# Kernel tuning notes

Measured on AMD Instinct MI355X. Metric: run time of the kernel, lower is better.

## Reference

```python
import jax, jax.numpy as jnp
import numpy as np

B, N, H, W = 1, 256, 32, 32
C_LIDAR, C_RGB, K, S = 64, 64, 16, 3
MLP3 = [128, 64, 64]


def _l2norm(x, eps=1e-12):
    n = jnp.linalg.norm(x, axis=-1, keepdims=True)
    return x / jnp.maximum(n, eps)


def _cal_sim(src, dst):
    # src [B,N,C], dst [B,M,C] -> [B,N,M,2] (cosine sim normalized two ways)
    s = _l2norm(src)
    d = _l2norm(dst)
    sim = jnp.einsum('bmc,bnc->bmn', d, s)  # [B,M,N]
    dst_src = sim / (jnp.max(sim, axis=2, keepdims=True) + 1e-10)
    src_dst = jnp.swapaxes(sim, 1, 2)       # [B,N,M]
    src_dst = src_dst / (jnp.max(src_dst, axis=2, keepdims=True) + 1e-6)
    return jnp.stack([src_dst, jnp.swapaxes(dst_src, 1, 2)], axis=-1)


def _mlp(x, layers):
    # 1x1 conv + (identity-init BN folded) + ReLU chain, channel-last
    for w, b in layers:
        x = jax.nn.relu(x @ w + b)
    return x


def _unfold(x, s):
    # F.unfold with zero pad s//2: [B,C,H,W] -> [B, H*W, s*s, C]
    p = s // 2
    b, c, h, w = x.shape
    xp = jnp.pad(x, ((0, 0), (0, 0), (p, p), (p, p)))
    pats = jnp.stack([xp[:, :, i:i + h, j:j + w] for i in range(s) for j in range(s)], axis=2)
    return pats.reshape(b, c, s * s, h * w).transpose(0, 3, 2, 1)


def _weighted_pnp(src_xyz, uv, wgt):
    # weighted SVD (Kabsch) head: lift uv to 3D at source depth, solve R,t
    z = src_xyz[..., 2:3]
    dst = jnp.concatenate([uv, jnp.ones_like(z)], axis=-1) * z
    wn = wgt / (jnp.sum(wgt, axis=-1, keepdims=True) + 1e-8)
    sc = jnp.einsum('bn,bnc->bc', wn, src_xyz)
    dc = jnp.einsum('bn,bnc->bc', wn, dst)
    s_c = src_xyz - sc[:, None]
    d_c = dst - dc[:, None]
    Hm = jnp.einsum('bn,bni,bnj->bij', wn, s_c, d_c)
    U, _, Vt = jnp.linalg.svd(Hm)
    V = jnp.swapaxes(Vt, -1, -2)
    det = jnp.linalg.det(jnp.einsum('bik,bjk->bij', V, U))
    diag = jnp.stack([jnp.ones_like(det), jnp.ones_like(det), det], axis=-1)
    R = jnp.einsum('bik,bk,bjk->bij', V, diag, U)
    t = dc - jnp.einsum('bij,bj->bi', R, sc)
    return R, t


def reference(warped_xyz, warped_points, RF3, RF3_index, lidar_z,
              w2_0, b2_0, w2_1, b2_1, w2_2, b2_2,
              w3_0, b3_0, w3_1, b3_1, w3_2, b3_2,
              w1_0, b1_0, w1_1, b1_1, w1_2, b1_2,
              wm_0, bm_0, wm_1, bm_1, wm_2, bm_2):
    b, n, _ = warped_xyz.shape
    _, ci, h, w = RF3.shape
    m = h * w
    xyz = warped_xyz * lidar_z                       # [B,N,3]
    rf = RF3.transpose(0, 2, 3, 1).reshape(b, m, ci)   # [B,M,Ci]
    rfi = RF3_index.transpose(0, 2, 3, 1).reshape(b, m, 3)

    src_dst_sim = _cal_sim(warped_points, rf)        # [B,N,M,2]

    # kNN grouping of the point cloud onto itself
    d2 = jnp.sum((xyz[:, :, None, :] - xyz[:, None, :, :]) ** 2, axis=-1)
    _, idx = jax.lax.top_k(-d2, K)                   # [B,N,K]
    gather = jax.vmap(lambda pts, i: pts[i])
    pc_xyz_g = gather(xyz, idx)                      # [B,N,K,3]
    pc_pts_g = gather(warped_points, idx)            # [B,N,K,C]
    diff = pc_xyz_g - xyz[:, :, None, :]
    dn = jnp.linalg.norm(diff, axis=-1, keepdims=True)
    pc_nbr = jnp.concatenate([pc_pts_g, diff, dn], axis=-1)
    wts = _mlp(pc_nbr, [(w2_0, b2_0), (w2_1, b2_1), (w2_2, b2_2)])
    wts = jnp.max(wts, axis=-1, keepdims=True)
    wts = jax.nn.softmax(wts, axis=-2)
    pc_feats = jnp.sum(wts * pc_pts_g, axis=-2)      # [B,N,C]

    # image 3x3 neighbor grouping via unfold
    rf_nbr_idx = _unfold(RF3_index, S)               # [B,M,SS,3]
    rf_nbr_pts = _unfold(RF3, S)                     # [B,M,SS,Ci]
    iw = _mlp(jnp.concatenate([rf_nbr_idx, rf_nbr_pts], axis=-1),
              [(w3_0, b3_0), (w3_1, b3_1), (w3_2, b3_2)])
    iw = jnp.max(iw, axis=-1, keepdims=True)
    iw = jax.nn.softmax(iw, axis=-2)
    img_feats = jnp.sum(iw * rf_nbr_pts, axis=-2)    # [B,M,Ci]

    nbr_sim = _cal_sim(pc_feats, img_feats)          # [B,N,M,2]

    feats = jnp.concatenate([
        jnp.broadcast_to(xyz[:, :, None, :], (b, n, m, 3)),
        jnp.broadcast_to(rfi[:, None, :, :], (b, n, m, 3)),
        jnp.broadcast_to(warped_points[:, :, None, :], (b, n, m, warped_points.shape[-1])),
        jnp.broadcast_to(rf[:, None, :, :], (b, n, m, ci)),
        src_dst_sim, nbr_sim], axis=-1)              # [B,N,M,6+C+Ci+4]
    feats = _mlp(feats, [(w1_0, b1_0), (w1_1, b1_1), (w1_2, b1_2)])

    aw = jax.nn.softmax(jnp.max(feats, axis=-1), axis=-1)   # [B,N,M]
    corres_uv1 = jnp.einsum('bnm,bmc->bnc', aw, rfi)         # [B,N,3]
    att = jnp.einsum('bnm,bnmc->bnc', aw, feats)             # [B,N,64]
    att = _mlp(att, [(wm_0, bm_0), (wm_1, bm_1)])
    logits = att @ wm_2 + bm_2                               # [B,N,2]
    weights = jax.nn.softmax(logits, axis=-1)
    w_in = jnp.argmax(weights, axis=-1).astype(weights.dtype)
    R, t = _weighted_pnp(xyz, corres_uv1[..., :2], w_in)
    return R, t, weights


def setup_inputs():
    key = jax.random.key(0)
    ks = jax.random.split(key, 32)
    f32 = jnp.float32
    inp = {}
    inp['warped_xyz'] = jax.random.normal(ks[0], (B, N, 3), f32)
    inp['warped_points'] = jax.random.normal(ks[1], (B, N, C_LIDAR), f32)
    inp['RF3'] = jax.random.normal(ks[2], (B, C_RGB, H, W), f32)
    inp['RF3_index'] = jax.random.normal(ks[3], (B, 3, H, W), f32)
    inp['lidar_z'] = jax.random.uniform(ks[4], (B, N, 1), f32, 0.5, 2.0)
    wdims = {'w2_0': (4 + C_LIDAR, C_LIDAR), 'w2_1': (C_LIDAR, C_LIDAR), 'w2_2': (C_LIDAR, C_LIDAR),
             'w3_0': (3 + C_RGB, C_RGB), 'w3_1': (C_RGB, C_RGB), 'w3_2': (C_RGB, C_RGB),
             'w1_0': (6 + C_RGB + C_LIDAR + 4, MLP3[0]), 'w1_1': (MLP3[0], MLP3[1]), 'w1_2': (MLP3[1], MLP3[2]),
             'wm_0': (MLP3[2], MLP3[2]), 'wm_1': (MLP3[2], MLP3[0]), 'wm_2': (MLP3[0], 2)}
    for i, (name, d) in enumerate(wdims.items()):
        inp[name] = jax.random.normal(ks[5 + i], d, f32) * 0.05
        inp['b' + name[1:]] = jnp.zeros((d[1],), f32)
    return inp
```

## Files before the change

kernel.cpp:

```cpp
#include <hip/hip_runtime.h>
#include <math.h>


typedef _Float16 f16;
typedef __attribute__((ext_vector_type(4))) _Float16 f16x4;
typedef __attribute__((ext_vector_type(8))) _Float16 f16x8;
typedef __attribute__((ext_vector_type(4))) float f32x4;

constexpr int WS_XYZ  = 0;
constexpr int WS_RF   = 768;
constexpr int WS_RFI  = WS_RF   + 65536;
constexpr int WS_SN   = WS_RFI  + 3072;
constexpr int WS_RS   = WS_SN;
constexpr int WS_RD   = WS_SN   + 256;
constexpr int WS_DN   = WS_SN   + 16384;
constexpr int WS_SIM1 = WS_DN   + 65536;
constexpr int WS_RM1  = WS_SIM1 + 262144;
constexpr int WS_CM1  = WS_RM1  + 1024;
constexpr int WS_PCF  = WS_CM1  + 256;
constexpr int WS_IMGF = WS_PCF  + 16384;
constexpr int WS_PCN  = WS_IMGF + 65536;
constexpr int WS_IMGN = WS_PCN  + 16384;
constexpr int WS_SIM2 = WS_IMGN + 65536;
constexpr int WS_RM2  = WS_SIM2 + 262144;
constexpr int WS_CM2  = WS_RM2  + 1024;
constexpr int WS_B1   = WS_CM2  + 256;
constexpr int WS_B2   = WS_B1   + 32768;
constexpr int WS_ATT  = WS_B2   + 131072;
constexpr int WS_UV   = WS_ATT  + 16384;
constexpr int WS_WIN  = WS_UV   + 768;
constexpr int WS_KNN  = WS_WIN  + 256;
constexpr int WS_PM   = WS_KNN  + 4096;
constexpr int WS_PS   = WS_PM   + 2048;
constexpr int WS_PATT = WS_PS   + 2048;
constexpr int WS_PUV  = WS_PATT + 131072;
constexpr int WS_W11T = WS_PUV  + 6144;
constexpr int WS_W12T = WS_W11T + 4096;
constexpr int WS_G3   = WS_W12T + 2048;
constexpr int WS_SIMF = WS_G3   + 65600;

__global__ __launch_bounds__(256) void prep_kernel(float* ws, const float* wxyz,
                                                   const float* lz, const float* RF3,
                                                   const float* RFI, const float* w11,
                                                   const float* w12, const float* wpts) {
    int b = blockIdx.x;
    if (b < 319) {
        int i = b * 256 + threadIdx.x;
        if (i < 768) {
            int n = i / 3;
            ws[WS_XYZ + i] = wxyz[i] * lz[n];
        } else if (i < 768 + 65536) {
            int j = i - 768; int mm = j >> 6, c = j & 63;
            ws[WS_RF + j] = RF3[c * 1024 + mm];
        } else if (i < 768 + 65536 + 3072) {
            int j = i - (768 + 65536); int mm = j / 3, c = j - mm * 3;
            ws[WS_RFI + j] = RFI[c * 1024 + mm];
        } else if (i < 69376 + 8192) {
            int j = i - 69376; int col = j >> 7, k = j & 127;
            ((f16*)(ws + WS_W11T))[col * 128 + k] = (f16)w11[k * 64 + col];
        } else if (i < 69376 + 12288) {
            int j = i - (69376 + 8192); int col = j >> 6, k = j & 63;
            ((f16*)(ws + WS_W12T))[col * 64 + k] = (f16)w12[k * 64 + col];
        }
    } else if (b == 319) {
        int n = threadIdx.x;
        float s = 0.f;
        for (int c = 0; c < 64; c++) { float v = wpts[n * 64 + c]; s += v * v; }
        ws[WS_RS + n] = 1.f / fmaxf(sqrtf(s), 1e-12f);
    } else {
        int m = (b - 320) * 256 + threadIdx.x;
        float s = 0.f;
        for (int c = 0; c < 64; c++) { float v = RF3[c * 1024 + m]; s += v * v; }
        ws[WS_RD + m] = 1.f / fmaxf(sqrtf(s), 1e-12f);
    }
}

__global__ __launch_bounds__(256) void mid_kernel(float* ws, const float* wpts,
        const float* w30, const float* b30, const float* w10, const float* b10) {
    int b = blockIdx.x, t = threadIdx.x;
    __shared__ float px[256], py[256], pz[256], d2[256];
    __shared__ float rv[256];
    __shared__ int   ri[256];
    __shared__ float wred[4];
    if (b < 1024) {
        int m = b;
        int wave = t >> 6, lane = t & 63;
        const float* rf = ws + WS_RF;
        if (t < 64) px[t] = rf[m * 64 + t];
        __syncthreads();
        float acc = 0.f;
        const float4* sp = (const float4*)(wpts + t * 64);
        const float4* dp = (const float4*)px;
        for (int i = 0; i < 16; i++) {
            float4 s4 = sp[i], d4 = dp[i];
            acc += s4.x * d4.x + s4.y * d4.y + s4.z * d4.z + s4.w * d4.w;
        }
        acc = acc * ws[WS_RD + m] * ws[WS_RS + t];
        ws[WS_SIM1 + m * 256 + t] = acc;
        float mx = acc;
        for (int o = 32; o > 0; o >>= 1) mx = fmaxf(mx, __shfl_down(mx, o));
        if (lane == 0) wred[wave] = mx;
        __syncthreads();
        if (t == 0)
            ws[WS_RM1 + m] = fmaxf(fmaxf(wred[0], wred[1]), fmaxf(wred[2], wred[3]));
    } else if (b < 1281) {
        int m = (b - 1024) * 4 + (t >> 6), j = t & 63;
        if (m < 1025) {
            float acc;
            if (m < 1024) {
                float a0 = b30[j], a1 = 0.f, a2 = 0.f, a3 = 0.f;
                for (int i = 0; i < 3; i++) a0 += ws[WS_RFI + m * 3 + i] * w30[i * 64 + j];
                const float* rfm = ws + WS_RF + m * 64;
                const float* wp = w30 + 3 * 64 + j;
                for (int c = 0; c < 64; c += 4) {
                    a0 += rfm[c]     * wp[c * 64];
                    a1 += rfm[c + 1] * wp[(c + 1) * 64];
                    a2 += rfm[c + 2] * wp[(c + 2) * 64];
                    a3 += rfm[c + 3] * wp[(c + 3) * 64];
                }
                acc = (a0 + a1) + (a2 + a3);
            } else {
                acc = b30[j];
            }
            ws[WS_G3 + m * 64 + j] = fmaxf(acc, 0.f);
        }
    } else if (b < 1921) {
        int bb = (b - 1281) * 2 + (t >> 7);
        int j = t & 127;
        if (bb < 256) {
            int n = bb;
            float a0 = b10[j], a1 = 0.f, a2 = 0.f, a3 = 0.f;
            for (int i = 0; i < 3; i++) a0 += ws[WS_XYZ + n * 3 + i] * w10[i * 128 + j];
            const float* xp = wpts + n * 64;
            const float* wp = w10 + 6 * 128 + j;
            for (int c = 0; c < 64; c += 4) {
                a0 += xp[c]     * wp[c * 128];
                a1 += xp[c + 1] * wp[(c + 1) * 128];
                a2 += xp[c + 2] * wp[(c + 2) * 128];
                a3 += xp[c + 3] * wp[(c + 3) * 128];
            }
            ws[WS_B1 + n * 128 + j] = (a0 + a1) + (a2 + a3);
        } else {
            int m = bb - 256;
            float a0 = 0.f, a1 = 0.f, a2 = 0.f, a3 = 0.f;
            for (int i = 0; i < 3; i++) a0 += ws[WS_RFI + m * 3 + i] * w10[(3 + i) * 128 + j];
            const float* rfm = ws + WS_RF + m * 64;
            const float* wp = w10 + 70 * 128 + j;
            for (int c = 0; c < 64; c += 4) {
                a0 += rfm[c]     * wp[c * 128];
                a1 += rfm[c + 1] * wp[(c + 1) * 128];
                a2 += rfm[c + 2] * wp[(c + 2) * 128];
                a3 += rfm[c + 3] * wp[(c + 3) * 128];
            }
            ws[WS_B2 + m * 128 + j] = (a0 + a1) + (a2 + a3);
        }
    } else {
        const float* xyz = ws + WS_XYZ;
        int* knn = (int*)(ws + WS_KNN);
        int n = b - 1921;
        px[t] = xyz[t * 3 + 0]; py[t] = xyz[t * 3 + 1]; pz[t] = xyz[t * 3 + 2];
        __syncthreads();
        float dx = px[t] - px[n], dy = py[t] - py[n], dz = pz[t] - pz[n];
        d2[t] = dx * dx + dy * dy + dz * dz;
        __syncthreads();
        for (int k = 0; k < 16; k++) {
            rv[t] = d2[t]; ri[t] = t;
            __syncthreads();
            for (int s = 128; s > 0; s >>= 1) {
                if (t < s) {
                    float v2 = rv[t + s]; int i2 = ri[t + s];
                    if (v2 < rv[t] || (v2 == rv[t] && i2 < ri[t])) { rv[t] = v2; ri[t] = i2; }
                }
                __syncthreads();
            }
            if (t == 0) { knn[n * 16 + k] = ri[0]; d2[ri[0]] = INFINITY; }
            __syncthreads();
        }
    }
}

__global__ __launch_bounds__(256) void sim2_kernel(float* ws) {
    __shared__ __align__(16) float dv[64];
    __shared__ float wred[4];
    int m = blockIdx.x, t = threadIdx.x;
    int wave = t >> 6, lane = t & 63;
    if (t < 64) dv[t] = ws[WS_IMGN + m * 64 + t];
    __syncthreads();
    float acc = 0.f;
    const float4* sp = (const float4*)(ws + WS_PCN + t * 64);
    const float4* dp = (const float4*)dv;
    for (int i = 0; i < 16; i++) {
        float4 s4 = sp[i], d4 = dp[i];
        acc += s4.x * d4.x + s4.y * d4.y + s4.z * d4.z + s4.w * d4.w;
    }
    ws[WS_SIM2 + m * 256 + t] = acc;
    float mx = acc;
    for (int o = 32; o > 0; o >>= 1) mx = fmaxf(mx, __shfl_down(mx, o));
    if (lane == 0) wred[wave] = mx;
    __syncthreads();
    if (t == 0)
        ws[WS_RM2 + m] = fmaxf(fmaxf(wred[0], wred[1]), fmaxf(wred[2], wred[3]));
}

__global__ __launch_bounds__(256) void simfeat_kernel(float* ws) {
    __shared__ float wred1[4], wred2[4];
    int n = blockIdx.x, t = threadIdx.x;
    int wave = t >> 6, lane = t & 63;
    const float* sim1 = ws + WS_SIM1;  const float* rm1g = ws + WS_RM1;
    const float* sim2 = ws + WS_SIM2;  const float* rm2g = ws + WS_RM2;
    f16* simfg = (f16*)(ws + WS_SIMF);
    float s1v[4], s2v[4];
    float mx1 = -INFINITY, mx2 = -INFINITY;
    for (int j = 0; j < 4; j++) {
        int m = t + j * 256;
        s1v[j] = sim1[m * 256 + n]; mx1 = fmaxf(mx1, s1v[j]);
        s2v[j] = sim2[m * 256 + n]; mx2 = fmaxf(mx2, s2v[j]);
    }
    float m1 = mx1, m2 = mx2;
    for (int o = 32; o > 0; o >>= 1) {
        m1 = fmaxf(m1, __shfl_down(m1, o));
        m2 = fmaxf(m2, __shfl_down(m2, o));
    }
    if (lane == 0) { wred1[wave] = m1; wred2[wave] = m2; }
    __syncthreads();
    float cm1 = fmaxf(fmaxf(wred1[0], wred1[1]), fmaxf(wred1[2], wred1[3]));
    float cm2 = fmaxf(fmaxf(wred2[0], wred2[1]), fmaxf(wred2[2], wred2[3]));
    for (int j = 0; j < 4; j++) {
        int m = t + j * 256;
        float r1 = rm1g[m], r2 = rm2g[m];
        float f0 = s1v[j] / (cm1 + 1e-6f);
        float f1 = s1v[j] / (r1 + 1e-10f);
        float f2 = s2v[j] / (cm2 + 1e-6f);
        float f3 = s2v[j] / (r2 + 1e-10f);
        *(f16x4*)&simfg[(n * 1024 + m) * 4] =
            (f16x4){(f16)f0, (f16)f1, (f16)f2, (f16)f3};
    }
}

__global__ __launch_bounds__(256) void mlp23_kernel(float* ws, const float* wpts,
        const float* w20, const float* b20, const float* w21, const float* b21,
        const float* w22, const float* b22,
        const float* w31, const float* b31, const float* w32, const float* b32) {
    __shared__ float sbuf[36 * 68 * 2];
    __shared__ float small1[36], small2[36];
    __shared__ int   kn[16];
    int b = blockIdx.x, t = threadIdx.x;
    if (b < 256) {
        int n = b;
        float* x  = sbuf;
        float* hA = sbuf + 1088;
        float* hB = sbuf + 2176;
        const float* xyz = ws + WS_XYZ;
        const int* knn = (const int*)(ws + WS_KNN);
        if (t < 16) kn[t] = knn[n * 16 + t];
        __syncthreads();
        for (int i = t; i < 1024; i += 256) {
            int k = i >> 6, c = i & 63;
            x[k * 68 + c] = wpts[kn[k] * 64 + c];
        }
        if (t < 16) {
            int i = kn[t];
            float dx = xyz[i * 3 + 0] - xyz[n * 3 + 0];
            float dy = xyz[i * 3 + 1] - xyz[n * 3 + 1];
            float dz = xyz[i * 3 + 2] - xyz[n * 3 + 2];
            x[t * 68 + 64] = dx; x[t * 68 + 65] = dy; x[t * 68 + 66] = dz;
            x[t * 68 + 67] = sqrtf(dx * dx + dy * dy + dz * dz);
        }
        __syncthreads();
        for (int o = t; o < 1024; o += 256) {
            int k = o >> 6, j = o & 63;
            float a0 = b20[j], a1 = 0.f, a2 = 0.f, a3 = 0.f;
            const float* xr = &x[k * 68];
            const float* wp = w20 + j;
            for (int i = 0; i < 68; i += 4) {
                a0 += xr[i]     * wp[i * 64];
                a1 += xr[i + 1] * wp[(i + 1) * 64];
                a2 += xr[i + 2] * wp[(i + 2) * 64];
                a3 += xr[i + 3] * wp[(i + 3) * 64];
            }
            hA[k * 68 + j] = fmaxf((a0 + a1) + (a2 + a3), 0.f);
        }
        __syncthreads();
        for (int o = t; o < 1024; o += 256) {
            int k = o >> 6, j = o & 63;
            float a0 = b21[j], a1 = 0.f, a2 = 0.f, a3 = 0.f;
            const float* xr = &hA[k * 68];
            const float* wp = w21 + j;
            for (int i = 0; i < 64; i += 4) {
                a0 += xr[i]     * wp[i * 64];
                a1 += xr[i + 1] * wp[(i + 1) * 64];
                a2 += xr[i + 2] * wp[(i + 2) * 64];
                a3 += xr[i + 3] * wp[(i + 3) * 64];
            }
            hB[k * 68 + j] = fmaxf((a0 + a1) + (a2 + a3), 0.f);
        }
        __syncthreads();
        for (int o = t; o < 1024; o += 256) {
            int k = o >> 6, j = o & 63;
            float a0 = b22[j], a1 = 0.f, a2 = 0.f, a3 = 0.f;
            const float* xr = &hB[k * 68];
            const float* wp = w22 + j;
            for (int i = 0; i < 64; i += 4) {
                a0 += xr[i]     * wp[i * 64];
                a1 += xr[i + 1] * wp[(i + 1) * 64];
                a2 += xr[i + 2] * wp[(i + 2) * 64];
                a3 += xr[i + 3] * wp[(i + 3) * 64];
            }
            hA[k * 68 + j] = fmaxf((a0 + a1) + (a2 + a3), 0.f);
        }
        __syncthreads();
        if (t < 16) {
            float mx = -INFINITY;
            for (int j = 0; j < 64; j++) mx = fmaxf(mx, hA[t * 68 + j]);
            small1[t] = mx;
        }
        __syncthreads();
        if (t < 16) {
            float mx = -INFINITY;
            for (int k = 0; k < 16; k++) mx = fmaxf(mx, small1[k]);
            float sum = 0.f;
            for (int k = 0; k < 16; k++) sum += expf(small1[k] - mx);
            small2[t] = expf(small1[t] - mx) / sum;
        }
        __syncthreads();
        if (t < 64) {
            float acc = 0.f;
            for (int k = 0; k < 16; k++) acc += small2[k] * x[k * 68 + t];
            float s = acc * acc;
            for (int o = 32; o > 0; o >>= 1) s += __shfl_down(s, o);
            s = __shfl(s, 0);
            ws[WS_PCN + n * 64 + t] = acc / fmaxf(sqrtf(s), 1e-12f);
        }
    } else {
        int m0 = (b - 256) * 4;
        float* x1 = sbuf;
        float* h2 = sbuf + 2448;
        const float* G = ws + WS_G3;
        const float* rf = ws + WS_RF;
        for (int i = t; i < 36 * 64; i += 256) {
            int row = i >> 6, c = i & 63;
            int mi = row / 9, kk = row - mi * 9;
            int m = m0 + mi; int y = m >> 5, x = m & 31;
            int dy = kk / 3 - 1, dx = kk % 3 - 1;
            int ny = y + dy, nx = x + dx;
            bool val = (ny >= 0 && ny < 32 && nx >= 0 && nx < 32);
            int idx = val ? (ny * 32 + nx) : 1024;
            x1[row * 68 + c] = G[idx * 64 + c];
        }
        __syncthreads();
        for (int o = t; o < 36 * 64; o += 256) {
            int row = o >> 6, c = o & 63;
            float a0 = b31[c], a1 = 0.f, a2 = 0.f, a3 = 0.f;
            const float* xr = &x1[row * 68];
            const float* wp = w31 + c;
            for (int i = 0; i < 64; i += 4) {
                a0 += xr[i]     * wp[i * 64];
                a1 += xr[i + 1] * wp[(i + 1) * 64];
                a2 += xr[i + 2] * wp[(i + 2) * 64];
                a3 += xr[i + 3] * wp[(i + 3) * 64];
            }
            h2[row * 68 + c] = fmaxf((a0 + a1) + (a2 + a3), 0.f);
        }
        __syncthreads();
        for (int o = t; o < 36 * 64; o += 256) {
            int row = o >> 6, c = o & 63;
            float a0 = b32[c], a1 = 0.f, a2 = 0.f, a3 = 0.f;
            const float* xr = &h2[row * 68];
            const float* wp = w32 + c;
            for (int i = 0; i < 64; i += 4) {
                a0 += xr[i]     * wp[i * 64];
                a1 += xr[i + 1] * wp[(i + 1) * 64];
                a2 += xr[i + 2] * wp[(i + 2) * 64];
                a3 += xr[i + 3] * wp[(i + 3) * 64];
            }
            x1[row * 68 + c] = fmaxf((a0 + a1) + (a2 + a3), 0.f);
        }
        __syncthreads();
        if (t < 36) {
            float mx = -INFINITY;
            for (int c = 0; c < 64; c++) mx = fmaxf(mx, x1[t * 68 + c]);
            small1[t] = mx;
        }
        __syncthreads();
        if (t < 36) {
            int mi = t / 9;
            float mx = -INFINITY;
            for (int k = 0; k < 9; k++) mx = fmaxf(mx, small1[mi * 9 + k]);
            float sum = 0.f;
            for (int k = 0; k < 9; k++) sum += expf(small1[mi * 9 + k] - mx);
            small2[t] = expf(small1[t] - mx) / sum;
        }
        __syncthreads();
        {
            int mi = t >> 6, c = t & 63;
            int m = m0 + mi; int y = m >> 5, x = m & 31;
            float acc = 0.f;
            for (int kk = 0; kk < 9; kk++) {
                int dy = kk / 3 - 1, dx = kk % 3 - 1;
                int ny = y + dy, nx = x + dx;
                bool val = (ny >= 0 && ny < 32 && nx >= 0 && nx < 32);
                if (val) acc += small2[mi * 9 + kk] * rf[(ny * 32 + nx) * 64 + c];
            }
            float s = acc * acc;
            for (int o = 32; o > 0; o >>= 1) s += __shfl_down(s, o);
            s = __shfl(s, 0);
            ws[WS_IMGN + m * 64 + c] = acc / fmaxf(sqrtf(s), 1e-12f);
        }
    }
}

__global__ __launch_bounds__(256) void mlp1_kernel(float* ws, const float* w10,
        const float* b11, const float* b12) {
    __shared__ __align__(16) f16 H1h[64 * 136];
    __shared__ __align__(16) f16 H2h[64 * 72];
    __shared__ float base1n[128];
    __shared__ float simw[4 * 128];
    __shared__ float rmPart[4][64];
    int n = blockIdx.y, seg = blockIdx.x, t = threadIdx.x;
    int wave = t >> 6, lane = t & 63, q = lane >> 4, l16 = lane & 15;
    int col = wave * 16 + l16;
    const float* base2 = ws + WS_B2;
    const float* rfig = ws + WS_RFI;
    const f16* simfg = (const f16*)(ws + WS_SIMF);
    const f16* w11t = (const f16*)(ws + WS_W11T);
    const f16* w12t = (const f16*)(ws + WS_W12T);
    if (t < 128) base1n[t] = ws[WS_B1 + n * 128 + t];
    for (int i = t; i < 512; i += 256) simw[i] = w10[134 * 128 + i];
    f16x8 B2f[4], B3f[2];
    for (int s = 0; s < 4; s++) B2f[s] = *(const f16x8*)&w11t[col * 128 + s * 32 + q * 8];
    for (int s = 0; s < 2; s++) B3f[s] = *(const f16x8*)&w12t[col * 64 + s * 32 + q * 8];
    float bias2 = b11[col], bias3 = b12[col];
    float attAcc = 0.f;
    float uv0 = 0.f, uv1 = 0.f, uv2 = 0.f;
    float Mv = -INFINITY, Sv = 0.f;
    int mBeg = seg * 128;
    __syncthreads();
    for (int c4 = 0; c4 < 2; c4++) {
        int m0 = mBeg + c4 * 64;
        for (int idx = t; idx < 2048; idx += 256) {
            int row = idx >> 5, k4 = (idx & 31) * 4;
            int m = m0 + row;
            f16x4 sf = *(const f16x4*)&simfg[(n * 1024 + m) * 4];
            float s0 = (float)sf[0], s1 = (float)sf[1], s2 = (float)sf[2], s3 = (float)sf[3];
            float4 bs = *(const float4*)&base2[m * 128 + k4];
            float4 b1v = *(const float4*)&base1n[k4];
            float4 w0v = *(const float4*)&simw[k4];
            float4 w1v = *(const float4*)&simw[128 + k4];
            float4 w2v = *(const float4*)&simw[256 + k4];
            float4 w3v = *(const float4*)&simw[384 + k4];
            float v0 = b1v.x + bs.x + s0 * w0v.x + s1 * w1v.x + s2 * w2v.x + s3 * w3v.x;
            float v1 = b1v.y + bs.y + s0 * w0v.y + s1 * w1v.y + s2 * w2v.y + s3 * w3v.y;
            float v2 = b1v.z + bs.z + s0 * w0v.z + s1 * w1v.z + s2 * w2v.z + s3 * w3v.z;
            float v3 = b1v.w + bs.w + s0 * w0v.w + s1 * w1v.w + s2 * w2v.w + s3 * w3v.w;
            *(f16x4*)&H1h[row * 136 + k4] = (f16x4){
                (f16)fmaxf(v0, 0.f), (f16)fmaxf(v1, 0.f),
                (f16)fmaxf(v2, 0.f), (f16)fmaxf(v3, 0.f)};
        }
        __syncthreads();
        f32x4 a[4];
        for (int tl = 0; tl < 4; tl++) a[tl] = (f32x4){bias2, bias2, bias2, bias2};
        for (int s = 0; s < 4; s++)
            for (int tl = 0; tl < 4; tl++) {
                f16x8 f = *(const f16x8*)&H1h[(tl * 16 + l16) * 136 + s * 32 + q * 8];
                a[tl] = __builtin_amdgcn_mfma_f32_16x16x32_f16(f, B2f[s], a[tl], 0, 0, 0);
            }
        for (int tl = 0; tl < 4; tl++)
            for (int r = 0; r < 4; r++)
                H2h[(tl * 16 + q * 4 + r) * 72 + col] = (f16)fmaxf(a[tl][r], 0.f);
        __syncthreads();
        f32x4 c3[4];
        for (int tl = 0; tl < 4; tl++) c3[tl] = (f32x4){bias3, bias3, bias3, bias3};
        for (int s = 0; s < 2; s++)
            for (int tl = 0; tl < 4; tl++) {
                f16x8 f = *(const f16x8*)&H2h[(tl * 16 + l16) * 72 + s * 32 + q * 8];
                c3[tl] = __builtin_amdgcn_mfma_f32_16x16x32_f16(f, B3f[s], c3[tl], 0, 0, 0);
            }
        for (int tl = 0; tl < 4; tl++)
            for (int r = 0; r < 4; r++)
                c3[tl][r] = fmaxf(c3[tl][r], 0.f);
        for (int tl = 0; tl < 4; tl++)
            for (int r = 0; r < 4; r++) {
                float v = c3[tl][r];
                v = fmaxf(v, __shfl_xor(v, 1));
                v = fmaxf(v, __shfl_xor(v, 2));
                v = fmaxf(v, __shfl_xor(v, 4));
                v = fmaxf(v, __shfl_xor(v, 8));
                if (l16 == 0) rmPart[wave][tl * 16 + q * 4 + r] = v;
            }
        __syncthreads();
        float rmv = fmaxf(fmaxf(rmPart[0][lane], rmPart[1][lane]),
                          fmaxf(rmPart[2][lane], rmPart[3][lane]));
        float tv = rmv;
        for (int off = 32; off > 0; off >>= 1) tv = fmaxf(tv, __shfl_xor(tv, off));
        float newM = fmaxf(Mv, tv);
        float rescale = __expf(Mv - newM);
        float ewv = __expf(rmv - newM);
        Mv = newM;
        float se = ewv;
        for (int off = 32; off > 0; off >>= 1) se += __shfl_xor(se, off);
        Sv = Sv * rescale + se;
        float ap = 0.f;
        for (int tl = 0; tl < 4; tl++)
            for (int r = 0; r < 4; r++)
                ap += __shfl(ewv, tl * 16 + q * 4 + r) * c3[tl][r];
        ap += __shfl_xor(ap, 16);
        ap += __shfl_xor(ap, 32);
        if (lane < 16) attAcc = attAcc * rescale + ap;
        if (wave == 0) {
            const float* rp = &rfig[(m0 + lane) * 3];
            float u0 = ewv * rp[0], u1 = ewv * rp[1], u2 = ewv * rp[2];
            for (int off = 32; off > 0; off >>= 1) {
                u0 += __shfl_xor(u0, off);
                u1 += __shfl_xor(u1, off);
                u2 += __shfl_xor(u2, off);
            }
            uv0 = uv0 * rescale + u0;
            uv1 = uv1 * rescale + u1;
            uv2 = uv2 * rescale + u2;
        }
    }
    int p = n * 8 + seg;
    if (t == 0) {
        ws[WS_PM + p] = Mv; ws[WS_PS + p] = Sv;
        ws[WS_PUV + p * 3 + 0] = uv0;
        ws[WS_PUV + p * 3 + 1] = uv1;
        ws[WS_PUV + p * 3 + 2] = uv2;
    }
    if (lane < 16) ws[WS_PATT + p * 64 + wave * 16 + lane] = attAcc;
}

__global__ __launch_bounds__(128) void combinehead_kernel(float* ws,
        const float* wm0, const float* bm0, const float* wm1, const float* bm1,
        const float* wm2, const float* bm2, float* out) {
    __shared__ float av[64], ha[64], hb[128], lg[2];
    int n = blockIdx.x, t = threadIdx.x;
    float pm[8], e[8];
    float M = -INFINITY;
    for (int s = 0; s < 8; s++) { pm[s] = ws[WS_PM + n * 8 + s]; M = fmaxf(M, pm[s]); }
    float S = 0.f;
    for (int s = 0; s < 8; s++) { e[s] = expf(pm[s] - M); S += ws[WS_PS + n * 8 + s] * e[s]; }
    if (t < 64) {
        float acc = 0.f;
        for (int s = 0; s < 8; s++) acc += ws[WS_PATT + (n * 8 + s) * 64 + t] * e[s];
        av[t] = acc / S;
    } else if (t < 67) {
        int c = t - 64; float acc = 0.f;
        for (int s = 0; s < 8; s++) acc += ws[WS_PUV + (n * 8 + s) * 3 + c] * e[s];
        ws[WS_UV + n * 3 + c] = acc / S;
    }
    __syncthreads();
    if (t < 64) {
        float acc = bm0[t];
        for (int i = 0; i < 64; i++) acc += av[i] * wm0[i * 64 + t];
        ha[t] = fmaxf(acc, 0.f);
    }
    __syncthreads();
    {
        float acc = bm1[t];
        for (int i = 0; i < 64; i++) acc += ha[i] * wm1[i * 128 + t];
        hb[t] = fmaxf(acc, 0.f);
    }
    __syncthreads();
    if (t < 2) {
        float acc = bm2[t];
        for (int i = 0; i < 128; i++) acc += hb[i] * wm2[i * 2 + t];
        lg[t] = acc;
    }
    __syncthreads();
    if (t == 0) {
        float l0 = lg[0], l1 = lg[1];
        float mx = fmaxf(l0, l1);
        float e0 = expf(l0 - mx), e1 = expf(l1 - mx);
        float s = e0 + e1;
        out[12 + n * 2 + 0] = e0 / s;
        out[12 + n * 2 + 1] = e1 / s;
        ws[WS_WIN + n] = (e1 > e0) ? 1.f : 0.f;
    }
}

__device__ void compute_rt(const double Hm[9], const double sc[3], const double dc[3],
                           float* out) {
    double Hd[3][3] = {{Hm[0], Hm[1], Hm[2]}, {Hm[3], Hm[4], Hm[5]}, {Hm[6], Hm[7], Hm[8]}};
    double A[3][3], V[3][3] = {{1, 0, 0}, {0, 1, 0}, {0, 0, 1}};
    for (int i = 0; i < 3; i++)
        for (int j = 0; j < 3; j++) {
            double s = 0;
            for (int k = 0; k < 3; k++) s += Hd[k][i] * Hd[k][j];
            A[i][j] = s;
        }
    for (int sweep = 0; sweep < 50; sweep++) {
        double off = fabs(A[0][1]) + fabs(A[0][2]) + fabs(A[1][2]);
        if (off < 1e-28) break;
        const int PQ[3][2] = {{0, 1}, {0, 2}, {1, 2}};
        for (int pp = 0; pp < 3; pp++) {
            int p = PQ[pp][0], q = PQ[pp][1];
            double apq = A[p][q];
            if (fabs(apq) < 1e-300) continue;
            double tau = (A[q][q] - A[p][p]) / (2.0 * apq);
            double tt = (tau >= 0.0 ? 1.0 : -1.0) / (fabs(tau) + sqrt(1.0 + tau * tau));
            double c = 1.0 / sqrt(1.0 + tt * tt), s = tt * c;
            for (int k = 0; k < 3; k++) {
                double akp = A[k][p], akq = A[k][q];
                A[k][p] = c * akp - s * akq; A[k][q] = s * akp + c * akq;
            }
            for (int k = 0; k < 3; k++) {
                double apk = A[p][k], aqk = A[q][k];
                A[p][k] = c * apk - s * aqk; A[q][k] = s * apk + c * aqk;
            }
            for (int k = 0; k < 3; k++) {
                double vkp = V[k][p], vkq = V[k][q];
                V[k][p] = c * vkp - s * vkq; V[k][q] = s * vkp + c * vkq;
            }
        }
    }
    double lam[3] = {A[0][0], A[1][1], A[2][2]};
    int o0 = 0, o1 = 1, o2 = 2;
    if (lam[o0] < lam[o1]) { int tp = o0; o0 = o1; o1 = tp; }
    if (lam[o0] < lam[o2]) { int tp = o0; o0 = o2; o2 = tp; }
    if (lam[o1] < lam[o2]) { int tp = o1; o1 = o2; o2 = tp; }
    int ord[3] = {o0, o1, o2};
    double v[3][3], u[3][3], R[3][3];
    for (int k = 0; k < 3; k++)
        for (int i = 0; i < 3; i++) v[k][i] = V[i][ord[k]];
    double sv0 = sqrt(fmax(lam[o0], 0.0));
    if (!(sv0 > 1e-150)) {
        for (int i = 0; i < 3; i++)
            for (int j = 0; j < 3; j++) R[i][j] = (i == j) ? 1.0 : 0.0;
    } else {
        double nn[3];
        for (int k = 0; k < 3; k++) {
            for (int i = 0; i < 3; i++)
                u[k][i] = Hd[i][0] * v[k][0] + Hd[i][1] * v[k][1] + Hd[i][2] * v[k][2];
            nn[k] = sqrt(u[k][0] * u[k][0] + u[k][1] * u[k][1] + u[k][2] * u[k][2]);
        }
        for (int i = 0; i < 3; i++) u[0][i] /= nn[0];
        if (nn[1] > 1e-12 * nn[0]) {
            for (int i = 0; i < 3; i++) u[1][i] /= nn[1];
        } else {
            int e = (fabs(u[0][0]) <= fabs(u[0][1]) && fabs(u[0][0]) <= fabs(u[0][2])) ? 0
                    : ((fabs(u[0][1]) <= fabs(u[0][2])) ? 1 : 2);
            double ev[3] = {0, 0, 0}; ev[e] = 1.0;
            double d0 = ev[0] * u[0][0] + ev[1] * u[0][1] + ev[2] * u[0][2];
            double w1v[3], wn2 = 0;
            for (int i = 0; i < 3; i++) { w1v[i] = ev[i] - d0 * u[0][i]; wn2 += w1v[i] * w1v[i]; }
            wn2 = sqrt(wn2);
            for (int i = 0; i < 3; i++) u[1][i] = w1v[i] / wn2;
        }
        if (nn[2] > 1e-10 * nn[0]) {
            for (int i = 0; i < 3; i++) u[2][i] /= nn[2];
        } else {
            u[2][0] = u[0][1] * u[1][2] - u[0][2] * u[1][1];
            u[2][1] = u[0][2] * u[1][0] - u[0][0] * u[1][2];
            u[2][2] = u[0][0] * u[1][1] - u[0][1] * u[1][0];
        }
        double cr[3] = {u[1][1] * u[2][2] - u[1][2] * u[2][1],
                        u[1][2] * u[2][0] - u[1][0] * u[2][2],
                        u[1][0] * u[2][1] - u[1][1] * u[2][0]};
        double detU = u[0][0] * cr[0] + u[0][1] * cr[1] + u[0][2] * cr[2];
        double cv[3] = {v[1][1] * v[2][2] - v[1][2] * v[2][1],
                        v[1][2] * v[2][0] - v[1][0] * v[2][2],
                        v[1][0] * v[2][1] - v[1][1] * v[2][0]};
        double detV = v[0][0] * cv[0] + v[0][1] * cv[1] + v[0][2] * cv[2];
        double dsign = detU * detV;
        for (int i = 0; i < 3; i++)
            for (int j = 0; j < 3; j++)
                R[i][j] = v[0][i] * u[0][j] + v[1][i] * u[1][j] + dsign * v[2][i] * u[2][j];
    }
    for (int i = 0; i < 3; i++) {
        double ti = dc[i] - (R[i][0] * sc[0] + R[i][1] * sc[1] + R[i][2] * sc[2]);
        out[9 + i] = (float)ti;
        for (int j = 0; j < 3; j++) out[i * 3 + j] = (float)R[i][j];
    }
}

__global__ __launch_bounds__(256) void pnp_kernel(float* ws, float* out) {
    __shared__ double red[9][256];
    int t = threadIdx.x;
    double w = (double)ws[WS_WIN + t];
    double x0 = ws[WS_XYZ + t * 3 + 0];
    double x1 = ws[WS_XYZ + t * 3 + 1];
    double x2 = ws[WS_XYZ + t * 3 + 2];
    double z = x2;
    double dd0 = (double)ws[WS_UV + t * 3 + 0] * z;
    double dd1 = (double)ws[WS_UV + t * 3 + 1] * z;
    double dd2 = z;
    red[0][t] = w;
    red[1][t] = w * x0; red[2][t] = w * x1; red[3][t] = w * x2;
    red[4][t] = w * dd0; red[5][t] = w * dd1; red[6][t] = w * dd2;
    __syncthreads();
    for (int s = 128; s > 0; s >>= 1) {
        if (t < s)
            for (int k = 0; k < 7; k++) red[k][t] += red[k][t + s];
        __syncthreads();
    }
    double wsum = red[0][0];
    double sx0 = red[1][0], sx1 = red[2][0], sx2 = red[3][0];
    double sd0 = red[4][0], sd1 = red[5][0], sd2 = red[6][0];
    __syncthreads();
    double inv = 1.0 / (wsum + 1e-8);
    double sc[3] = {sx0 * inv, sx1 * inv, sx2 * inv};
    double dc[3] = {sd0 * inv, sd1 * inv, sd2 * inv};
    double wn = w * inv;
    double a0 = x0 - sc[0], a1 = x1 - sc[1], a2 = x2 - sc[2];
    double b0 = dd0 - dc[0], b1 = dd1 - dc[1], b2 = dd2 - dc[2];
    red[0][t] = wn * a0 * b0; red[1][t] = wn * a0 * b1; red[2][t] = wn * a0 * b2;
    red[3][t] = wn * a1 * b0; red[4][t] = wn * a1 * b1; red[5][t] = wn * a1 * b2;
    red[6][t] = wn * a2 * b0; red[7][t] = wn * a2 * b1; red[8][t] = wn * a2 * b2;
    __syncthreads();
    for (int s = 128; s > 0; s >>= 1) {
        if (t < s)
            for (int k = 0; k < 9; k++) red[k][t] += red[k][t + s];
        __syncthreads();
    }
    if (t == 0) {
        double Hm[9];
        for (int k = 0; k < 9; k++) Hm[k] = red[k][0];
        compute_rt(Hm, sc, dc, out);
    }
}

extern "C" void kernel_launch(void* const* d_in, const int* in_sizes, int n_in,
                              void* d_out, int out_size, void* d_ws, size_t ws_size,
                              hipStream_t stream) {
    float* ws = (float*)d_ws;
    const float* wxyz = (const float*)d_in[0];
    const float* wpts = (const float*)d_in[1];
    const float* RF3  = (const float*)d_in[2];
    const float* RFI  = (const float*)d_in[3];
    const float* lz   = (const float*)d_in[4];
    const float* w2_0 = (const float*)d_in[5];  const float* b2_0 = (const float*)d_in[6];
    const float* w2_1 = (const float*)d_in[7];  const float* b2_1 = (const float*)d_in[8];
    const float* w2_2 = (const float*)d_in[9];  const float* b2_2 = (const float*)d_in[10];
    const float* w3_0 = (const float*)d_in[11]; const float* b3_0 = (const float*)d_in[12];
    const float* w3_1 = (const float*)d_in[13]; const float* b3_1 = (const float*)d_in[14];
    const float* w3_2 = (const float*)d_in[15]; const float* b3_2 = (const float*)d_in[16];
    const float* w1_0 = (const float*)d_in[17]; const float* b1_0 = (const float*)d_in[18];
    const float* w1_1 = (const float*)d_in[19]; const float* b1_1 = (const float*)d_in[20];
    const float* w1_2 = (const float*)d_in[21]; const float* b1_2 = (const float*)d_in[22];
    const float* wm_0 = (const float*)d_in[23]; const float* bm_0 = (const float*)d_in[24];
    const float* wm_1 = (const float*)d_in[25]; const float* bm_1 = (const float*)d_in[26];
    const float* wm_2 = (const float*)d_in[27]; const float* bm_2 = (const float*)d_in[28];
    float* out = (float*)d_out;

    prep_kernel<<<324, 256, 0, stream>>>(ws, wxyz, lz, RF3, RFI, w1_1, w1_2, wpts);
    mid_kernel<<<2177, 256, 0, stream>>>(ws, wpts, w3_0, b3_0, w1_0, b1_0);
    mlp23_kernel<<<512, 256, 0, stream>>>(ws, wpts, w2_0, b2_0, w2_1, b2_1, w2_2, b2_2,
                                          w3_1, b3_1, w3_2, b3_2);
    sim2_kernel<<<1024, 256, 0, stream>>>(ws);
    simfeat_kernel<<<256, 256, 0, stream>>>(ws);
    mlp1_kernel<<<dim3(8, 256), 256, 0, stream>>>(ws, w1_0, b1_1, b1_2);
    combinehead_kernel<<<256, 128, 0, stream>>>(ws, wm_0, bm_0, wm_1, bm_1, wm_2, bm_2, out);
    pnp_kernel<<<1, 256, 0, stream>>>(ws, out);
}
```

Measured before the change: 236.4 us.

## Transpose point features and similarity matrices for coalesced access

Adds a transposed copy of the point features built in prep_kernel and writes the normalized point features transposed, so the sim1/sim2 dot products read channel-major data that is coalesced across threads instead of strided rows. The similarity matrices are stored as [n][m], so simfeat_kernel reads them contiguously rather than with a 256-float stride. Adds 64 prep blocks and changes layouts shared by several kernels, so any other consumer of the old WS_PCN or similarity layout would now read stale or misordered data.

```diff
diff --git a/kernel.cpp b/kernel.cpp
--- a/kernel.cpp
+++ b/kernel.cpp
@@ -13,12 +13,12 @@
 constexpr int WS_SN   = WS_RFI  + 3072;
 constexpr int WS_RS   = WS_SN;
 constexpr int WS_RD   = WS_SN   + 256;
-constexpr int WS_DN   = WS_SN   + 16384;
-constexpr int WS_SIM1 = WS_DN   + 65536;
+constexpr int WS_WPT  = WS_SN   + 16384;
+constexpr int WS_SIM1 = WS_WPT  + 65536;
 constexpr int WS_RM1  = WS_SIM1 + 262144;
 constexpr int WS_CM1  = WS_RM1  + 1024;
-constexpr int WS_PCF  = WS_CM1  + 256;
-constexpr int WS_IMGF = WS_PCF  + 16384;
+constexpr int WS_PCT  = WS_CM1  + 256;
+constexpr int WS_IMGF = WS_PCT  + 16384;
 constexpr int WS_PCN  = WS_IMGF + 65536;
 constexpr int WS_IMGN = WS_PCN  + 16384;
 constexpr int WS_SIM2 = WS_IMGN + 65536;
@@ -67,11 +67,15 @@
         float s = 0.f;
         for (int c = 0; c < 64; c++) { float v = wpts[n * 64 + c]; s += v * v; }
         ws[WS_RS + n] = 1.f / fmaxf(sqrtf(s), 1e-12f);
-    } else {
+    } else if (b < 324) {
         int m = (b - 320) * 256 + threadIdx.x;
         float s = 0.f;
         for (int c = 0; c < 64; c++) { float v = RF3[c * 1024 + m]; s += v * v; }
         ws[WS_RD + m] = 1.f / fmaxf(sqrtf(s), 1e-12f);
+    } else {
+        int i = (b - 324) * 256 + threadIdx.x;
+        int c = i >> 8, n = i & 255;
+        ws[WS_WPT + c * 256 + n] = wpts[n * 64 + c];
     }
 }
 
@@ -86,17 +90,18 @@
         int m = b;
         int wave = t >> 6, lane = t & 63;
         const float* rf = ws + WS_RF;
+        const float* wptsT = ws + WS_WPT;
         if (t < 64) px[t] = rf[m * 64 + t];
         __syncthreads();
         float acc = 0.f;
-        const float4* sp = (const float4*)(wpts + t * 64);
-        const float4* dp = (const float4*)px;
-        for (int i = 0; i < 16; i++) {
-            float4 s4 = sp[i], d4 = dp[i];
-            acc += s4.x * d4.x + s4.y * d4.y + s4.z * d4.z + s4.w * d4.w;
+        for (int c = 0; c < 64; c += 4) {
+            acc += px[c]     * wptsT[c * 256 + t]
+                 + px[c + 1] * wptsT[(c + 1) * 256 + t]
+                 + px[c + 2] * wptsT[(c + 2) * 256 + t]
+                 + px[c + 3] * wptsT[(c + 3) * 256 + t];
         }
         acc = acc * ws[WS_RD + m] * ws[WS_RS + t];
-        ws[WS_SIM1 + m * 256 + t] = acc;
+        ws[WS_SIM1 + t * 1024 + m] = acc;
         float mx = acc;
         for (int o = 32; o > 0; o >>= 1) mx = fmaxf(mx, __shfl_down(mx, o));
         if (lane == 0) wred[wave] = mx;
@@ -186,14 +191,15 @@
     int wave = t >> 6, lane = t & 63;
     if (t < 64) dv[t] = ws[WS_IMGN + m * 64 + t];
     __syncthreads();
+    const float* pcnT = ws + WS_PCT;
     float acc = 0.f;
-    const float4* sp = (const float4*)(ws + WS_PCN + t * 64);
-    const float4* dp = (const float4*)dv;
-    for (int i = 0; i < 16; i++) {
-        float4 s4 = sp[i], d4 = dp[i];
-        acc += s4.x * d4.x + s4.y * d4.y + s4.z * d4.z + s4.w * d4.w;
-    }
-    ws[WS_SIM2 + m * 256 + t] = acc;
+    for (int c = 0; c < 64; c += 4) {
+        acc += dv[c]     * pcnT[c * 256 + t]
+             + dv[c + 1] * pcnT[(c + 1) * 256 + t]
+             + dv[c + 2] * pcnT[(c + 2) * 256 + t]
+             + dv[c + 3] * pcnT[(c + 3) * 256 + t];
+    }
+    ws[WS_SIM2 + t * 1024 + m] = acc;
     float mx = acc;
     for (int o = 32; o > 0; o >>= 1) mx = fmaxf(mx, __shfl_down(mx, o));
     if (lane == 0) wred[wave] = mx;
@@ -213,8 +219,8 @@
     float mx1 = -INFINITY, mx2 = -INFINITY;
     for (int j = 0; j < 4; j++) {
         int m = t + j * 256;
-        s1v[j] = sim1[m * 256 + n]; mx1 = fmaxf(mx1, s1v[j]);
-        s2v[j] = sim2[m * 256 + n]; mx2 = fmaxf(mx2, s2v[j]);
+        s1v[j] = sim1[n * 1024 + m]; mx1 = fmaxf(mx1, s1v[j]);
+        s2v[j] = sim2[n * 1024 + m]; mx2 = fmaxf(mx2, s2v[j]);
     }
     float m1 = mx1, m2 = mx2;
     for (int o = 32; o > 0; o >>= 1) {
@@ -329,7 +335,7 @@
             float s = acc * acc;
             for (int o = 32; o > 0; o >>= 1) s += __shfl_down(s, o);
             s = __shfl(s, 0);
-            ws[WS_PCN + n * 64 + t] = acc / fmaxf(sqrtf(s), 1e-12f);
+            ws[WS_PCT + t * 256 + n] = acc / fmaxf(sqrtf(s), 1e-12f);
         }
     } else {
         int m0 = (b - 256) * 4;
@@ -742,7 +748,7 @@
     const float* wm_2 = (const float*)d_in[27]; const float* bm_2 = (const float*)d_in[28];
     float* out = (float*)d_out;
 
-    prep_kernel<<<324, 256, 0, stream>>>(ws, wxyz, lz, RF3, RFI, w1_1, w1_2, wpts);
+    prep_kernel<<<388, 256, 0, stream>>>(ws, wxyz, lz, RF3, RFI, w1_1, w1_2, wpts);
     mid_kernel<<<2177, 256, 0, stream>>>(ws, wpts, w3_0, b3_0, w1_0, b1_0);
     mlp23_kernel<<<512, 256, 0, stream>>>(ws, wpts, w2_0, b2_0, w2_1, b2_1, w2_2, b2_2,
                                           w3_1, b3_1, w3_2, b3_2);
```

After: 223.3 us (median of 2 runs). 1.06x faster.
